# Kernel tuning notes

Hardware: AMD Instinct MI355X
Metric: run time of the kernel (lower is better)

Reference implementation:

```python
import jax, jax.numpy as jnp
import numpy as np

N = 50000      # nodes
F_IN = 128     # num_feat
HID = 128      # hidden size
OUT = 47       # num_out (classes)
E = 600000     # graph edges
EGO_E = 1200000  # concatenated egonet edges


def _linear_params(key, fan_in, fan_out):
    s = 1.0 / np.sqrt(fan_in)
    kw, kb = jax.random.split(key)
    W = jax.random.uniform(kw, (fan_in, fan_out), jnp.float32, -s, s)
    b = jax.random.uniform(kb, (fan_out,), jnp.float32, -s, s)
    return W, b


def setup_inputs() -> dict:
    key = jax.random.key(0)
    ks = jax.random.split(key, 8)
    x_in = jax.random.normal(ks[0], (N, F_IN), jnp.float32)
    edge_index_in = jax.random.randint(ks[1], (2, E), 0, N)
    ego_edge_index = jax.random.randint(ks[2], (2, EGO_E), 0, N)
    W_ego0, b_ego0 = _linear_params(ks[3], F_IN, F_IN)
    W_gin0, b_gin0 = _linear_params(ks[4], F_IN, HID)
    W_ego1, b_ego1 = _linear_params(ks[5], HID, HID)
    W_gin1, b_gin1 = _linear_params(ks[6], HID, OUT)
    return {
        "x_in": x_in, "edge_index_in": edge_index_in, "ego_edge_index": ego_edge_index,
        "W_ego0": W_ego0, "b_ego0": b_ego0, "W_gin0": W_gin0, "b_gin0": b_gin0,
        "W_ego1": W_ego1, "b_ego1": b_ego1, "W_gin1": W_gin1, "b_gin1": b_gin1,
    }


def reference(x_in, edge_index_in, ego_edge_index,
              W_ego0, b_ego0, W_gin0, b_gin0,
              W_ego1, b_ego1, W_gin1, b_gin1):
    n = x_in.shape[0]
    ego_row, ego_col = ego_edge_index[0], ego_edge_index[1]
    src, tgt = edge_index_in[0], edge_index_in[1]

    def do_conv(x):
        # sum_i spmm(A_i, x) == scatter-add over concatenated egonet edges, then / N
        return jax.ops.segment_sum(x[ego_col], ego_row, num_segments=n) * (1.0 / n)

    def gin(x, W, b):
        # GINConv(nn=Linear), eps=0: Linear(x + sum_{j->i} x_j)
        aggr = jax.ops.segment_sum(x[src], tgt, num_segments=n)
        return (x + aggr) @ W + b

    # layer 0: ['Ego','GIN', relu_mid=True, relu_end=True]
    x = do_conv(x_in) @ W_ego0 + b_ego0
    x = jax.nn.relu(x)
    x = gin(x, W_gin0, b_gin0)
    x = jax.nn.relu(x)
    # layer 1: ['Ego','GIN', relu_mid=True, relu_end=False]
    x = do_conv(x) @ W_ego1 + b_ego1
    x = jax.nn.relu(x)
    x = gin(x, W_gin1, b_gin1)
    return jax.nn.log_softmax(x, axis=1)
```

## Files before the change

kernel.cpp:

```cpp
#include <hip/hip_runtime.h>

#define SCAP_EGO 8192
#define SCAP_E   4096

typedef unsigned short ushort_t;
typedef unsigned int uint_t;
typedef __attribute__((ext_vector_type(8))) short bf16x8;
typedef __attribute__((ext_vector_type(4))) float f32x4;

__device__ inline float lo16(uint_t u) { return __uint_as_float(u << 16); }
__device__ inline float hi16(uint_t u) { return __uint_as_float(u & 0xFFFF0000u); }
__device__ inline ushort_t f2bf(float f) {
    uint_t i = __float_as_uint(f);
    return (ushort_t)((i + 0x7FFFu + ((i >> 16) & 1u)) >> 16);
}
__device__ inline uint_t pack2(float a, float b) {
    return (uint_t)f2bf(a) | ((uint_t)f2bf(b) << 16);
}
union U8 { uint4 u; bf16x8 v; };

__global__ __launch_bounds__(256) void prep(
    const float* __restrict__ x, ushort_t* __restrict__ xb, int n8,
    const float* __restrict__ W0, const float* __restrict__ W1,
    const float* __restrict__ W2, const float* __restrict__ W3,
    ushort_t* __restrict__ T0, ushort_t* __restrict__ T1,
    ushort_t* __restrict__ T2, ushort_t* __restrict__ T3,
    int* __restrict__ z)
{
    int i = blockIdx.x * 256 + threadIdx.x;
    if (i < 128) ((int4*)z)[i] = make_int4(0, 0, 0, 0);
    if (i < n8) {
        const float4* p = (const float4*)(x + (size_t)i * 8);
        float4 a = p[0], b = p[1];
        uint4 o;
        o.x = pack2(a.x, a.y); o.y = pack2(a.z, a.w);
        o.z = pack2(b.x, b.y); o.w = pack2(b.z, b.w);
        *(uint4*)(xb + (size_t)i * 8) = o;
    }
    if (i < 49152) {
        int mi = i >> 14;
        int r = i & 16383;
        int n = r >> 7, k = r & 127;
        const float* W = mi == 0 ? W0 : (mi == 1 ? W1 : W2);
        ushort_t* T = mi == 0 ? T0 : (mi == 1 ? T1 : T2);
        T[n * 128 + k] = f2bf(W[k * 128 + n]);
    } else if (i < 49152 + 6144) {
        int r = i - 49152;
        int n = r >> 7, k = r & 127;
        T3[n * 128 + k] = (n < 47) ? f2bf(W3[k * 47 + n]) : (ushort_t)0;
    }
}

__global__ __launch_bounds__(256) void bin_edges(
    const int* __restrict__ dst, const int* __restrict__ src, int nE, int scap,
    int* __restrict__ bincur, int2* __restrict__ stage)
{
    __shared__ int bcnt[256];
    __shared__ int gbase[256];
    int t = threadIdx.x;
    bcnt[t] = 0;
    __syncthreads();
    int base = blockIdx.x * 4096;
    int d[16], s[16], l[16];
#pragma unroll
    for (int i = 0; i < 16; i++) {
        int e = base + t + i * 256;
        if (e < nE) {
            d[i] = dst[e]; s[i] = src[e];
            l[i] = atomicAdd(&bcnt[d[i] >> 8], 1);
        } else d[i] = -1;
    }
    __syncthreads();
    if (bcnt[t]) gbase[t] = atomicAdd(&bincur[t], bcnt[t]);
    __syncthreads();
#pragma unroll
    for (int i = 0; i < 16; i++) {
        if (d[i] >= 0) {
            int b = d[i] >> 8;
            int slot = gbase[b] + l[i];
            if (slot < scap) stage[(size_t)b * scap + slot] = make_int2(d[i], s[i]);
        }
    }
}

__global__ __launch_bounds__(256) void build_csr(
    const int* __restrict__ bincur, const int2* __restrict__ stage, int scap,
    int* __restrict__ cnt, int* __restrict__ rowptr, int* __restrict__ packed,
    int nNodes)
{
    __shared__ int sc[256];
    __shared__ int wcur[256];
    int b = blockIdx.x, t = threadIdx.x;
    int m = bincur[b]; if (m > scap) m = scap;
    const int2* st = stage + (size_t)b * scap;
    sc[t] = 0;
    __syncthreads();
    for (int e = t; e < m; e += 256) atomicAdd(&sc[st[e].x & 255], 1);
    __syncthreads();
    int v = sc[t];
    __syncthreads();
    sc[t] = v;
    __syncthreads();
    for (int off = 1; off < 256; off <<= 1) {
        int y = (t >= off) ? sc[t - off] : 0;
        __syncthreads();
        sc[t] += y;
        __syncthreads();
    }
    int excl = sc[t] - v;
    int node = b * 256 + t;
    if (node < nNodes) { cnt[node] = v; rowptr[node] = b * scap + excl; }
    wcur[t] = excl;
    __syncthreads();
    int* pk = packed + (size_t)b * scap;
    for (int e = t; e < m; e += 256) {
        int2 p = st[e];
        int slot = atomicAdd(&wcur[p.x & 255], 1);
        pk[slot] = p.y;
    }
}

__global__ __launch_bounds__(256) void gather_bf(
    const ushort_t* __restrict__ x, const int* __restrict__ cnt,
    const int* __restrict__ rowptr, const int* __restrict__ packed,
    ushort_t* __restrict__ outb, int nNodes, float scale, int selfAdd)
{
    int g = threadIdx.x >> 4, lane = threadIdx.x & 15;
    int n = blockIdx.x * 16 + g;
    if (n >= nNodes) return;
    int len = cnt[n];
    const int* row = packed + rowptr[n];
    const ushort_t* base = x + lane * 8;
    float a[8];
#pragma unroll
    for (int m = 0; m < 8; m++) a[m] = 0.f;
    int e = 0;
    for (; e + 3 < len; e += 4) {
        int s0 = row[e], s1 = row[e + 1], s2 = row[e + 2], s3 = row[e + 3];
        uint4 w0 = *(const uint4*)(base + (size_t)s0 * 128);
        uint4 w1 = *(const uint4*)(base + (size_t)s1 * 128);
        uint4 w2 = *(const uint4*)(base + (size_t)s2 * 128);
        uint4 w3 = *(const uint4*)(base + (size_t)s3 * 128);
        a[0] += lo16(w0.x) + lo16(w1.x) + lo16(w2.x) + lo16(w3.x);
        a[1] += hi16(w0.x) + hi16(w1.x) + hi16(w2.x) + hi16(w3.x);
        a[2] += lo16(w0.y) + lo16(w1.y) + lo16(w2.y) + lo16(w3.y);
        a[3] += hi16(w0.y) + hi16(w1.y) + hi16(w2.y) + hi16(w3.y);
        a[4] += lo16(w0.z) + lo16(w1.z) + lo16(w2.z) + lo16(w3.z);
        a[5] += hi16(w0.z) + hi16(w1.z) + hi16(w2.z) + hi16(w3.z);
        a[6] += lo16(w0.w) + lo16(w1.w) + lo16(w2.w) + lo16(w3.w);
        a[7] += hi16(w0.w) + hi16(w1.w) + hi16(w2.w) + hi16(w3.w);
    }
    for (; e < len; e++) {
        uint4 w = *(const uint4*)(base + (size_t)row[e] * 128);
        a[0] += lo16(w.x); a[1] += hi16(w.x);
        a[2] += lo16(w.y); a[3] += hi16(w.y);
        a[4] += lo16(w.z); a[5] += hi16(w.z);
        a[6] += lo16(w.w); a[7] += hi16(w.w);
    }
    if (selfAdd) {
        uint4 w = *(const uint4*)(base + (size_t)n * 128);
        a[0] += lo16(w.x); a[1] += hi16(w.x);
        a[2] += lo16(w.y); a[3] += hi16(w.y);
        a[4] += lo16(w.z); a[5] += hi16(w.z);
        a[6] += lo16(w.w); a[7] += hi16(w.w);
    }
    uint4 o;
    o.x = pack2(a[0] * scale, a[1] * scale);
    o.y = pack2(a[2] * scale, a[3] * scale);
    o.z = pack2(a[4] * scale, a[5] * scale);
    o.w = pack2(a[6] * scale, a[7] * scale);
    *(uint4*)(outb + (size_t)n * 128 + lane * 8) = o;
}

template<bool RELU>
__global__ __launch_bounds__(256) void gemm_mfma(
    const ushort_t* __restrict__ A, const ushort_t* __restrict__ WT,
    const float* __restrict__ bias, ushort_t* __restrict__ outb, int nrows)
{
    __shared__ ushort_t Ws[128][136];
    int t = threadIdx.x;
    for (int j = t; j < 128 * 16; j += 256) {
        int n = j >> 4, kq = (j & 15) << 3;
        *(uint4*)&Ws[n][kq] = *(const uint4*)(WT + n * 128 + kq);
    }
    int wave = t >> 6, lane = t & 63;
    int m = lane & 15, quad = lane >> 4;
    int rowBase = blockIdx.x * 64 + wave * 16;
    int arow = rowBase + m; if (arow >= nrows) arow = 0;
    bf16x8 afr[4];
#pragma unroll
    for (int kt = 0; kt < 4; kt++) {
        U8 u; u.u = *(const uint4*)(A + (size_t)arow * 128 + kt * 32 + quad * 8);
        afr[kt] = u.v;
    }
    __syncthreads();
    f32x4 acc[8];
#pragma unroll
    for (int ct = 0; ct < 8; ct++) acc[ct] = (f32x4){0.f, 0.f, 0.f, 0.f};
#pragma unroll
    for (int ct = 0; ct < 8; ct++) {
#pragma unroll
        for (int kt = 0; kt < 4; kt++) {
            bf16x8 b = *(const bf16x8*)&Ws[ct * 16 + m][kt * 32 + quad * 8];
            acc[ct] = __builtin_amdgcn_mfma_f32_16x16x32_bf16(afr[kt], b, acc[ct], 0, 0, 0);
        }
    }
#pragma unroll
    for (int ct = 0; ct < 8; ct++) {
        int col = ct * 16 + m;
        float bb = bias[col];
#pragma unroll
        for (int r = 0; r < 4; r++) {
            int row = rowBase + quad * 4 + r;
            if (row < nrows) {
                float v = acc[ct][r] + bb;
                if (RELU) v = fmaxf(v, 0.f);
                outb[(size_t)row * 128 + col] = f2bf(v);
            }
        }
    }
}

__global__ __launch_bounds__(256) void gemm47_lsm(
    const ushort_t* __restrict__ A, const ushort_t* __restrict__ WT,
    const float* __restrict__ bias, float* __restrict__ out, int nrows)
{
    __shared__ ushort_t Ws[48][136];
    int t = threadIdx.x;
    for (int j = t; j < 48 * 16; j += 256) {
        int n = j >> 4, kq = (j & 15) << 3;
        *(uint4*)&Ws[n][kq] = *(const uint4*)(WT + n * 128 + kq);
    }
    int wave = t >> 6, lane = t & 63;
    int m = lane & 15, quad = lane >> 4;
    int rowBase = blockIdx.x * 64 + wave * 16;
    int arow = rowBase + m; if (arow >= nrows) arow = 0;
    bf16x8 afr[4];
#pragma unroll
    for (int kt = 0; kt < 4; kt++) {
        U8 u; u.u = *(const uint4*)(A + (size_t)arow * 128 + kt * 32 + quad * 8);
        afr[kt] = u.v;
    }
    __syncthreads();
    f32x4 acc[3];
#pragma unroll
    for (int ct = 0; ct < 3; ct++) acc[ct] = (f32x4){0.f, 0.f, 0.f, 0.f};
#pragma unroll
    for (int ct = 0; ct < 3; ct++) {
#pragma unroll
        for (int kt = 0; kt < 4; kt++) {
            bf16x8 b = *(const bf16x8*)&Ws[ct * 16 + m][kt * 32 + quad * 8];
            acc[ct] = __builtin_amdgcn_mfma_f32_16x16x32_bf16(afr[kt], b, acc[ct], 0, 0, 0);
        }
    }
    int c0 = m, c1 = 16 + m, c2 = 32 + m;
    bool has2 = (c2 < 47);
    float b0 = bias[c0], b1 = bias[c1], b2 = has2 ? bias[c2] : 0.f;
#pragma unroll
    for (int r = 0; r < 4; r++) {
        int row = rowBase + quad * 4 + r;
        float v0 = acc[0][r] + b0;
        float v1 = acc[1][r] + b1;
        float v2 = has2 ? (acc[2][r] + b2) : -INFINITY;
        float mx = fmaxf(fmaxf(v0, v1), v2);
#pragma unroll
        for (int off = 8; off; off >>= 1) mx = fmaxf(mx, __shfl_xor(mx, off, 64));
        float s = __expf(v0 - mx) + __expf(v1 - mx) + (has2 ? __expf(v2 - mx) : 0.f);
#pragma unroll
        for (int off = 8; off; off >>= 1) s += __shfl_xor(s, off, 64);
        float lse = mx + __logf(s);
        if (row < nrows) {
            float* o = out + (size_t)row * 47;
            o[c0] = v0 - lse;
            o[c1] = v1 - lse;
            if (has2) o[c2] = v2 - lse;
        }
    }
}

extern "C" void kernel_launch(void* const* d_in, const int* in_sizes, int n_in,
                              void* d_out, int out_size, void* d_ws, size_t ws_size,
                              hipStream_t stream) {
    const float* x_in   = (const float*)d_in[0];
    const int*   edge   = (const int*)d_in[1];
    const int*   ego    = (const int*)d_in[2];
    const float* W_ego0 = (const float*)d_in[3];
    const float* b_ego0 = (const float*)d_in[4];
    const float* W_gin0 = (const float*)d_in[5];
    const float* b_gin0 = (const float*)d_in[6];
    const float* W_ego1 = (const float*)d_in[7];
    const float* b_ego1 = (const float*)d_in[8];
    const float* W_gin1 = (const float*)d_in[9];
    const float* b_gin1 = (const float*)d_in[10];
    float* out = (float*)d_out;

    const int N     = in_sizes[0] / 128;
    const int E     = in_sizes[1] / 2;
    const int EGO_E = in_sizes[2] / 2;
    const float invN = 1.0f / (float)N;
    const int NB    = (N + 255) >> 8;

    const size_t NBELEM = (size_t)N * 128;
    ushort_t* Xb = (ushort_t*)d_ws;
    ushort_t* G  = Xb + NBELEM;
    ushort_t* H  = G + NBELEM;
    ushort_t* T0 = H + NBELEM;
    ushort_t* T1 = T0 + 16384;
    ushort_t* T2 = T1 + 16384;
    ushort_t* T3 = T2 + 16384;
    int* ip = (int*)(T3 + 6144);
    int* cnt_ego  = ip;              ip += N;
    int* rp_ego   = ip;              ip += N;
    int* cnt_edge = ip;              ip += N;
    int* rp_edge  = ip;              ip += N;
    int* bincur   = ip;              ip += 512;
    int2* stage_ego  = (int2*)ip;    ip += (size_t)NB * SCAP_EGO * 2;
    int*  pk_ego     = ip;           ip += (size_t)NB * SCAP_EGO;
    int2* stage_edge = (int2*)ip;    ip += (size_t)NB * SCAP_E * 2;
    int*  pk_edge    = ip;           ip += (size_t)NB * SCAP_E;

    const int gGemm   = (N + 63) / 64;
    const int gNode16 = (N + 15) / 16;
    const int gBinE   = (EGO_E + 4095) / 4096;
    const int gBinF   = (E + 4095) / 4096;
    const int gCvt    = ((N * 128 / 8) + 255) / 256;

    prep<<<gCvt, 256, 0, stream>>>(x_in, Xb, N * 128 / 8,
                                   W_ego0, W_gin0, W_ego1, W_gin1,
                                   T0, T1, T2, T3, bincur);
    bin_edges<<<gBinE, 256, 0, stream>>>(ego, ego + EGO_E, EGO_E, SCAP_EGO, bincur, stage_ego);
    bin_edges<<<gBinF, 256, 0, stream>>>(edge + E, edge, E, SCAP_E, bincur + 256, stage_edge);
    build_csr<<<NB, 256, 0, stream>>>(bincur, stage_ego, SCAP_EGO, cnt_ego, rp_ego, pk_ego, N);
    build_csr<<<NB, 256, 0, stream>>>(bincur + 256, stage_edge, SCAP_E, cnt_edge, rp_edge, pk_edge, N);

    gather_bf<<<gNode16, 256, 0, stream>>>(Xb, cnt_ego, rp_ego, pk_ego, G, N, invN, 0);
    gemm_mfma<true><<<gGemm, 256, 0, stream>>>(G, T0, b_ego0, H, N);
    gather_bf<<<gNode16, 256, 0, stream>>>(H, cnt_edge, rp_edge, pk_edge, G, N, 1.f, 1);
    gemm_mfma<true><<<gGemm, 256, 0, stream>>>(G, T1, b_gin0, H, N);
    gather_bf<<<gNode16, 256, 0, stream>>>(H, cnt_ego, rp_ego, pk_ego, G, N, invN, 0);
    gemm_mfma<true><<<gGemm, 256, 0, stream>>>(G, T2, b_ego1, H, N);
    gather_bf<<<gNode16, 256, 0, stream>>>(H, cnt_edge, rp_edge, pk_edge, G, N, 1.f, 1);
    gemm47_lsm<<<gGemm, 256, 0, stream>>>(G, T3, b_gin1, out, N);
}
```

Baseline: 330.1 us.

## Merge CSR build launches and degree-sort nodes within bins for balanced gather

Merges the two edge-binning launches and the two CSR-build launches into single kernels that pick their dataset by block index, cutting launch count. Each CSR-build block now bitonic-sorts its 256 nodes by degree and writes a remap table, so the gather kernel gives the 16 nodes in a block similar edge counts and wavefront divergence is reduced. The gather also gains an 8-way unrolled loop for more loads in flight. Costs are a bitonic sort in the build step, an extra remap load per node, and arrays padded to a multiple of 256 nodes.

```diff
diff --git a/kernel.cpp b/kernel.cpp
--- a/kernel.cpp
+++ b/kernel.cpp
@@ -51,16 +51,26 @@
     }
 }
 
-__global__ __launch_bounds__(256) void bin_edges(
-    const int* __restrict__ dst, const int* __restrict__ src, int nE, int scap,
-    int* __restrict__ bincur, int2* __restrict__ stage)
-{
+__global__ __launch_bounds__(256) void bin_edges2(
+    const int* __restrict__ d1, const int* __restrict__ s1, int n1, int nb1,
+    int* __restrict__ cur1, int2* __restrict__ st1, int scap1,
+    const int* __restrict__ d2, const int* __restrict__ s2, int n2,
+    int* __restrict__ cur2, int2* __restrict__ st2, int scap2)
+{
+    const int* dst; const int* src; int nE, scap; int* bincur; int2* stage; int bid;
+    if (blockIdx.x < (uint_t)nb1) {
+        dst = d1; src = s1; nE = n1; scap = scap1; bincur = cur1; stage = st1;
+        bid = blockIdx.x;
+    } else {
+        dst = d2; src = s2; nE = n2; scap = scap2; bincur = cur2; stage = st2;
+        bid = blockIdx.x - nb1;
+    }
     __shared__ int bcnt[256];
     __shared__ int gbase[256];
     int t = threadIdx.x;
     bcnt[t] = 0;
     __syncthreads();
-    int base = blockIdx.x * 4096;
+    int base = bid * 4096;
     int d[16], s[16], l[16];
 #pragma unroll
     for (int i = 0; i < 16; i++) {
@@ -83,14 +93,27 @@
     }
 }
 
-__global__ __launch_bounds__(256) void build_csr(
-    const int* __restrict__ bincur, const int2* __restrict__ stage, int scap,
-    int* __restrict__ cnt, int* __restrict__ rowptr, int* __restrict__ packed,
-    int nNodes)
-{
+__global__ __launch_bounds__(256) void build_csr2(
+    const int* __restrict__ cur1, const int2* __restrict__ st1, int scap1,
+    int* __restrict__ cnt1, int* __restrict__ rp1, int* __restrict__ pk1,
+    int* __restrict__ remap1,
+    const int* __restrict__ cur2, const int2* __restrict__ st2, int scap2,
+    int* __restrict__ cnt2, int* __restrict__ rp2, int* __restrict__ pk2,
+    int* __restrict__ remap2, int NB)
+{
+    const int* bincur; const int2* stage; int scap;
+    int* cnt; int* rowptr; int* packed; int* remap; int b;
+    if (blockIdx.x < (uint_t)NB) {
+        bincur = cur1; stage = st1; scap = scap1;
+        cnt = cnt1; rowptr = rp1; packed = pk1; remap = remap1; b = blockIdx.x;
+    } else {
+        bincur = cur2; stage = st2; scap = scap2;
+        cnt = cnt2; rowptr = rp2; packed = pk2; remap = remap2; b = blockIdx.x - NB;
+    }
     __shared__ int sc[256];
     __shared__ int wcur[256];
-    int b = blockIdx.x, t = threadIdx.x;
+    __shared__ uint_t key[256];
+    int t = threadIdx.x;
     int m = bincur[b]; if (m > scap) m = scap;
     const int2* st = stage + (size_t)b * scap;
     sc[t] = 0;
@@ -100,6 +123,7 @@
     int v = sc[t];
     __syncthreads();
     sc[t] = v;
+    key[t] = ((uint_t)v << 8) | (uint_t)t;
     __syncthreads();
     for (int off = 1; off < 256; off <<= 1) {
         int y = (t >= off) ? sc[t - off] : 0;
@@ -108,10 +132,22 @@
         __syncthreads();
     }
     int excl = sc[t] - v;
-    int node = b * 256 + t;
-    if (node < nNodes) { cnt[node] = v; rowptr[node] = b * scap + excl; }
+    cnt[b * 256 + t] = v;
+    rowptr[b * 256 + t] = b * scap + excl;
     wcur[t] = excl;
-    __syncthreads();
+    for (int k = 2; k <= 256; k <<= 1) {
+        for (int j = k >> 1; j > 0; j >>= 1) {
+            __syncthreads();
+            int ixj = t ^ j;
+            if (ixj > t) {
+                uint_t a = key[t], c = key[ixj];
+                bool dir = ((t & k) == 0);
+                if ((a > c) == dir) { key[t] = c; key[ixj] = a; }
+            }
+        }
+    }
+    __syncthreads();
+    remap[b * 256 + t] = b * 256 + (int)(key[t] & 255u);
     int* pk = packed + (size_t)b * scap;
     for (int e = t; e < m; e += 256) {
         int2 p = st[e];
@@ -123,10 +159,11 @@
 __global__ __launch_bounds__(256) void gather_bf(
     const ushort_t* __restrict__ x, const int* __restrict__ cnt,
     const int* __restrict__ rowptr, const int* __restrict__ packed,
-    ushort_t* __restrict__ outb, int nNodes, float scale, int selfAdd)
+    const int* __restrict__ remap, ushort_t* __restrict__ outb,
+    int nNodes, float scale, int selfAdd)
 {
     int g = threadIdx.x >> 4, lane = threadIdx.x & 15;
-    int n = blockIdx.x * 16 + g;
+    int n = remap[blockIdx.x * 16 + g];
     if (n >= nNodes) return;
     int len = cnt[n];
     const int* row = packed + rowptr[n];
@@ -135,12 +172,37 @@
 #pragma unroll
     for (int m = 0; m < 8; m++) a[m] = 0.f;
     int e = 0;
+    for (; e + 7 < len; e += 8) {
+        uint4 w0 = *(const uint4*)(base + (size_t)row[e + 0] * 128);
+        uint4 w1 = *(const uint4*)(base + (size_t)row[e + 1] * 128);
+        uint4 w2 = *(const uint4*)(base + (size_t)row[e + 2] * 128);
+        uint4 w3 = *(const uint4*)(base + (size_t)row[e + 3] * 128);
+        uint4 w4 = *(const uint4*)(base + (size_t)row[e + 4] * 128);
+        uint4 w5 = *(const uint4*)(base + (size_t)row[e + 5] * 128);
+        uint4 w6 = *(const uint4*)(base + (size_t)row[e + 6] * 128);
+        uint4 w7 = *(const uint4*)(base + (size_t)row[e + 7] * 128);
+        a[0] += (lo16(w0.x) + lo16(w1.x)) + (lo16(w2.x) + lo16(w3.x))
+              + (lo16(w4.x) + lo16(w5.x)) + (lo16(w6.x) + lo16(w7.x));
+        a[1] += (hi16(w0.x) + hi16(w1.x)) + (hi16(w2.x) + hi16(w3.x))
+              + (hi16(w4.x) + hi16(w5.x)) + (hi16(w6.x) + hi16(w7.x));
+        a[2] += (lo16(w0.y) + lo16(w1.y)) + (lo16(w2.y) + lo16(w3.y))
+              + (lo16(w4.y) + lo16(w5.y)) + (lo16(w6.y) + lo16(w7.y));
+        a[3] += (hi16(w0.y) + hi16(w1.y)) + (hi16(w2.y) + hi16(w3.y))
+              + (hi16(w4.y) + hi16(w5.y)) + (hi16(w6.y) + hi16(w7.y));
+        a[4] += (lo16(w0.z) + lo16(w1.z)) + (lo16(w2.z) + lo16(w3.z))
+              + (lo16(w4.z) + lo16(w5.z)) + (lo16(w6.z) + lo16(w7.z));
+        a[5] += (hi16(w0.z) + hi16(w1.z)) + (hi16(w2.z) + hi16(w3.z))
+              + (hi16(w4.z) + hi16(w5.z)) + (hi16(w6.z) + hi16(w7.z));
+        a[6] += (lo16(w0.w) + lo16(w1.w)) + (lo16(w2.w) + lo16(w3.w))
+              + (lo16(w4.w) + lo16(w5.w)) + (lo16(w6.w) + lo16(w7.w));
+        a[7] += (hi16(w0.w) + hi16(w1.w)) + (hi16(w2.w) + hi16(w3.w))
+              + (hi16(w4.w) + hi16(w5.w)) + (hi16(w6.w) + hi16(w7.w));
+    }
     for (; e + 3 < len; e += 4) {
-        int s0 = row[e], s1 = row[e + 1], s2 = row[e + 2], s3 = row[e + 3];
-        uint4 w0 = *(const uint4*)(base + (size_t)s0 * 128);
-        uint4 w1 = *(const uint4*)(base + (size_t)s1 * 128);
-        uint4 w2 = *(const uint4*)(base + (size_t)s2 * 128);
-        uint4 w3 = *(const uint4*)(base + (size_t)s3 * 128);
+        uint4 w0 = *(const uint4*)(base + (size_t)row[e + 0] * 128);
+        uint4 w1 = *(const uint4*)(base + (size_t)row[e + 1] * 128);
+        uint4 w2 = *(const uint4*)(base + (size_t)row[e + 2] * 128);
+        uint4 w3 = *(const uint4*)(base + (size_t)row[e + 3] * 128);
         a[0] += lo16(w0.x) + lo16(w1.x) + lo16(w2.x) + lo16(w3.x);
         a[1] += hi16(w0.x) + hi16(w1.x) + hi16(w2.x) + hi16(w3.x);
         a[2] += lo16(w0.y) + lo16(w1.y) + lo16(w2.y) + lo16(w3.y);
@@ -309,18 +371,20 @@
     ushort_t* T2 = T1 + 16384;
     ushort_t* T3 = T2 + 16384;
     int* ip = (int*)(T3 + 6144);
-    int* cnt_ego  = ip;              ip += N;
-    int* rp_ego   = ip;              ip += N;
-    int* cnt_edge = ip;              ip += N;
-    int* rp_edge  = ip;              ip += N;
-    int* bincur   = ip;              ip += 512;
+    int* cnt_ego   = ip;             ip += NB * 256;
+    int* rp_ego    = ip;             ip += NB * 256;
+    int* rm_ego    = ip;             ip += NB * 256;
+    int* cnt_edge  = ip;             ip += NB * 256;
+    int* rp_edge   = ip;             ip += NB * 256;
+    int* rm_edge   = ip;             ip += NB * 256;
+    int* bincur    = ip;             ip += 512;
     int2* stage_ego  = (int2*)ip;    ip += (size_t)NB * SCAP_EGO * 2;
     int*  pk_ego     = ip;           ip += (size_t)NB * SCAP_EGO;
     int2* stage_edge = (int2*)ip;    ip += (size_t)NB * SCAP_E * 2;
     int*  pk_edge    = ip;           ip += (size_t)NB * SCAP_E;
 
     const int gGemm   = (N + 63) / 64;
-    const int gNode16 = (N + 15) / 16;
+    const int gNode16 = (NB * 256) / 16;
     const int gBinE   = (EGO_E + 4095) / 4096;
     const int gBinF   = (E + 4095) / 4096;
     const int gCvt    = ((N * 128 / 8) + 255) / 256;
@@ -328,17 +392,19 @@
     prep<<<gCvt, 256, 0, stream>>>(x_in, Xb, N * 128 / 8,
                                    W_ego0, W_gin0, W_ego1, W_gin1,
                                    T0, T1, T2, T3, bincur);
-    bin_edges<<<gBinE, 256, 0, stream>>>(ego, ego + EGO_E, EGO_E, SCAP_EGO, bincur, stage_ego);
-    bin_edges<<<gBinF, 256, 0, stream>>>(edge + E, edge, E, SCAP_E, bincur + 256, stage_edge);
-    build_csr<<<NB, 256, 0, stream>>>(bincur, stage_ego, SCAP_EGO, cnt_ego, rp_ego, pk_ego, N);
-    build_csr<<<NB, 256, 0, stream>>>(bincur + 256, stage_edge, SCAP_E, cnt_edge, rp_edge, pk_edge, N);
-
-    gather_bf<<<gNode16, 256, 0, stream>>>(Xb, cnt_ego, rp_ego, pk_ego, G, N, invN, 0);
+    bin_edges2<<<gBinE + gBinF, 256, 0, stream>>>(
+        ego, ego + EGO_E, EGO_E, gBinE, bincur, stage_ego, SCAP_EGO,
+        edge + E, edge, E, bincur + 256, stage_edge, SCAP_E);
+    build_csr2<<<2 * NB, 256, 0, stream>>>(
+        bincur, stage_ego, SCAP_EGO, cnt_ego, rp_ego, pk_ego, rm_ego,
+        bincur + 256, stage_edge, SCAP_E, cnt_edge, rp_edge, pk_edge, rm_edge, NB);
+
+    gather_bf<<<gNode16, 256, 0, stream>>>(Xb, cnt_ego, rp_ego, pk_ego, rm_ego, G, N, invN, 0);
     gemm_mfma<true><<<gGemm, 256, 0, stream>>>(G, T0, b_ego0, H, N);
-    gather_bf<<<gNode16, 256, 0, stream>>>(H, cnt_edge, rp_edge, pk_edge, G, N, 1.f, 1);
+    gather_bf<<<gNode16, 256, 0, stream>>>(H, cnt_edge, rp_edge, pk_edge, rm_edge, G, N, 1.f, 1);
     gemm_mfma<true><<<gGemm, 256, 0, stream>>>(G, T1, b_gin0, H, N);
-    gather_bf<<<gNode16, 256, 0, stream>>>(H, cnt_ego, rp_ego, pk_ego, G, N, invN, 0);
+    gather_bf<<<gNode16, 256, 0, stream>>>(H, cnt_ego, rp_ego, pk_ego, rm_ego, G, N, invN, 0);
     gemm_mfma<true><<<gGemm, 256, 0, stream>>>(G, T2, b_ego1, H, N);
-    gather_bf<<<gNode16, 256, 0, stream>>>(H, cnt_edge, rp_edge, pk_edge, G, N, 1.f, 1);
+    gather_bf<<<gNode16, 256, 0, stream>>>(H, cnt_edge, rp_edge, pk_edge, rm_edge, G, N, 1.f, 1);
     gemm47_lsm<<<gGemm, 256, 0, stream>>>(G, T3, b_gin1, out, N);
 }
```

After: 333.7 us. Within noise of the previous version (+1.1%).
